# Optimization experiments

Hardware: AMD Instinct MI355X
Metric: run time of the kernel (lower is better)

The kernel has to match this reference:

```python
import jax, jax.numpy as jnp
import numpy as np

B, T, D, H, C = 256, 512, 128, 2048, 128

def setup_inputs() -> dict:
    key = jax.random.key(0)
    ks = jax.random.split(key, 4)
    def xavier(k, shape):
        fan_in, fan_out = shape
        a = jnp.sqrt(6.0 / (fan_in + fan_out))
        return jax.random.uniform(k, shape, jnp.float32, -a, a)
    return {
        "x": jax.random.randint(ks[0], (B, T), 0, D, dtype=jnp.int32),
        "W_hx": xavier(ks[1], (D, H)),
        "W_hh": xavier(ks[2], (H, H)),
        "W_ph": xavier(ks[3], (H, C)),
        "b_h": jnp.zeros((H,), jnp.float32),
        "b_p": jnp.zeros((C,), jnp.float32),
    }

def reference(x, W_hx, W_hh, W_ph, b_h, b_p):
    # one_hot(x) @ W_hx is just a row gather of W_hx (same math, no dense one-hot)
    xw = W_hx[x] + b_h            # [B, T, H]
    xw_t = jnp.swapaxes(xw, 0, 1)  # [T, B, H] for scan over time

    def step(h, xw_step):
        h_new = jnp.tanh(xw_step + h @ W_hh)
        return h_new, None

    h0 = jnp.zeros((B, H), xw.dtype)
    h_final, _ = jax.lax.scan(step, h0, xw_t)
    out = h_final @ W_ph + b_p    # [B, C]
    return out
```

## Files before the change

### kernel.cpp

```cpp
#include <hip/hip_runtime.h>
#include <hip/hip_fp16.h>

#define B_ 256
#define T_ 512
#define H_ 2048
#define C_ 128
#define ASTR 520
#define BSTR2 1030
#define POLLCAP 200000

#define WS_H0 (0u)
#define WS_H1 (1u << 20)
#define WS_BT (2u << 20)

typedef _Float16 half8 __attribute__((ext_vector_type(8)));
typedef float floatx4 __attribute__((ext_vector_type(4)));

__device__ unsigned g_sync[8192];
__device__ _Float16 g_fb[2][8][32][H_];


__device__ __forceinline__ half8 llc_load16(const _Float16* p) {
    union { unsigned long long u[2]; half8 h; } v;
    const unsigned long long* q = (const unsigned long long*)p;
    v.u[0] = __hip_atomic_load(q,     __ATOMIC_RELAXED, __HIP_MEMORY_SCOPE_AGENT);
    v.u[1] = __hip_atomic_load(q + 1, __ATOMIC_RELAXED, __HIP_MEMORY_SCOPE_AGENT);
    return v.h;
}

__device__ __forceinline__ int xcc_id() {
    int x;
    asm volatile("s_getreg_b32 %0, hwreg(HW_REG_XCC_ID)" : "=s"(x));
    return x & 7;
}

__device__ __forceinline__ void flag_inc(unsigned* p) {
    __hip_atomic_fetch_add(p, 1u, __ATOMIC_RELAXED, __HIP_MEMORY_SCOPE_AGENT);
}
__device__ __forceinline__ void flag_poll_ge(const unsigned* p, unsigned tgt) {
    int n = 0;
    while (__hip_atomic_load(p, __ATOMIC_RELAXED, __HIP_MEMORY_SCOPE_AGENT) < tgt
           && n < POLLCAP) { __builtin_amdgcn_s_sleep(2); ++n; }
}

__global__ void convert_whh(const float* __restrict__ W, _Float16* __restrict__ BT) {
    __shared__ float tile[64][65];
    const int kb = blockIdx.x * 64, nb = blockIdx.y * 64;
    const int tid = threadIdx.x;
    const int rc = tid & 63, rr = tid >> 6;
#pragma unroll
    for (int i = 0; i < 16; ++i)
        tile[i * 4 + rr][rc] = W[(size_t)(kb + i * 4 + rr) * H_ + nb + rc];
    __syncthreads();
    const int j = tid & 15, blk = (tid >> 4) & 1, nof = tid >> 5;
#pragma unroll
    for (int i = 0; i < 8; ++i) {
        int n = i * 8 + nof;
        _Float16 v0 = (_Float16)tile[blk * 32 + j][n];
        _Float16 v1 = (_Float16)tile[blk * 32 + 16 + j][n];
        unsigned pk = ((unsigned)__builtin_bit_cast(unsigned short, v1) << 16)
                    |  (unsigned)__builtin_bit_cast(unsigned short, v0);
        *(unsigned*)(BT + (size_t)(nb + n) * H_ + kb + blk * 32 + 2 * j) = pk;
    }
}

__global__ void init_h(const int* __restrict__ x, const float* __restrict__ W_hx,
                       const float* __restrict__ b_h, char* __restrict__ ws) {
    int idx = blockIdx.x * blockDim.x + threadIdx.x;
    if (idx < 8192) g_sync[idx] = 0;
    _Float16* h0 = (_Float16*)(ws + WS_H0);
    int b = idx >> 11, s = idx & (H_ - 1);
    int j = (s & ~31) + ((s & 31) >> 1) + ((s & 1) << 4);
    int xv = x[b * T_];
    h0[idx] = (_Float16)tanhf(W_hx[(size_t)xv * H_ + j] + b_h[j]);
}

#define AL(dst, blk) { const _Float16* _ab = ap + (blk) * 256;              \
    _Pragma("unroll") for (int u = 0; u < 8; ++u)                           \
        asm volatile("global_load_dwordx4 %0, %1, off offset:%2 sc0"        \
                     : "=v"(dst[u]) : "v"(_ab), "i"(u * 64)); }

#define AL2(Aa, Bb0, Bb1, q) {                                              \
    const _Float16* _a2 = ap2 + (q) * 128;                                  \
    const _Float16* _b0 = btp0 + (q) * 128;                                 \
    const _Float16* _b1 = btp1 + (q) * 128;                                 \
    _Pragma("unroll") for (int u = 0; u < 4; ++u)                           \
        asm volatile("global_load_dwordx4 %0, %1, off offset:%2 sc0"        \
                     : "=v"(Aa[u]) : "v"(_a2), "i"(u * 64));                \
    _Pragma("unroll") for (int u = 0; u < 4; ++u)                           \
        asm volatile("global_load_dwordx4 %0, %1, off offset:%2 sc0"        \
                     : "=v"(Bb0[u]) : "v"(_b0), "i"(u * 64));               \
    _Pragma("unroll") for (int u = 0; u < 4; ++u)                           \
        asm volatile("global_load_dwordx4 %0, %1, off offset:%2 sc0"        \
                     : "=v"(Bb1[u]) : "v"(_b1), "i"(u * 64)); }

#define VWAIT(n)                                                            \
    asm volatile("s_waitcnt vmcnt(" #n ")" ::: "memory");                   \
    __builtin_amdgcn_sched_barrier(0);

#define FC_LDS(src, blk)                                                    \
    _Pragma("unroll") for (int u = 0; u < 8; ++u) {                         \
        half8 b0v = *(const half8*)(bsp0 + ((blk) * 8 + u) * 32);           \
        half8 b1v = *(const half8*)(bsp1 + ((blk) * 8 + u) * 32);           \
        acc0 = __builtin_amdgcn_mfma_f32_16x16x32_f16(src[u], b0v, acc0, 0, 0, 0); \
        acc1 = __builtin_amdgcn_mfma_f32_16x16x32_f16(src[u], b1v, acc1, 0, 0, 0); \
    }

#define FC_REG(Aa, Bb0, Bb1)                                                \
    _Pragma("unroll") for (int u = 0; u < 4; ++u) {                         \
        acc0 = __builtin_amdgcn_mfma_f32_16x16x32_f16(Aa[u], Bb0[u], acc0, 0, 0, 0); \
        acc1 = __builtin_amdgcn_mfma_f32_16x16x32_f16(Aa[u], Bb1[u], acc1, 0, 0, 0); \
    }

#define POLLF(qq) {                                                         \
    int guard = 0;                                                          \
    for (;;) {                                                              \
        unsigned fvv = need;                                                \
        if (l < 4) fvv = __hip_atomic_load(&gflags[(rb * 16 + (qq) * 4 + l) * 4], \
                                           __ATOMIC_RELAXED, __HIP_MEMORY_SCOPE_AGENT); \
        if (__ballot(fvv >= need) == ~0ull) break;                          \
        if (++guard > POLLCAP) break;                                       \
        __builtin_amdgcn_s_sleep(2);                                        \
    } }

#define STAGE_LOAD(hb, qq, r) {                                             \
    const _Float16* sp = (hb) + (size_t)(rbr + srow) * H_ + (qq) * 512 + skb; \
    r[0] = llc_load16(sp);      r[1] = llc_load16(sp + 8);                  \
    r[2] = llc_load16(sp + 16); r[3] = llc_load16(sp + 24); }

#define STAGE_WRITE(buf, r) {                                               \
    _Float16* dp = Asl + (buf) * 16 * ASTR + srow * ASTR + skb;             \
    *(half8*)(dp)      = r[0]; *(half8*)(dp + 8)  = r[1];                   \
    *(half8*)(dp + 16) = r[2]; *(half8*)(dp + 24) = r[3]; }

#define COMPUTE(qq) {                                                       \
    const _Float16* ar  = Asl + ((qq) & 1) * 16 * ASTR + l15 * ASTR + kl;   \
    const _Float16* b0p = BT + (size_t)(cw + l15) * H_ + (qq) * 512 + kl;   \
    const _Float16* b1p = BT + (size_t)(cw + 16 + l15) * H_ + (qq) * 512 + kl; \
    _Pragma("unroll")                                                       \
    for (int i = 0; i < 16; ++i) {                                          \
        half8 a  = *(const half8*)(ar  + i * 32);                           \
        half8 b0 = *(const half8*)(b0p + i * 32);                           \
        half8 b1 = *(const half8*)(b1p + i * 32);                           \
        acc0 = __builtin_amdgcn_mfma_f32_16x16x32_f16(a, b0, acc0, 0, 0, 0);\
        acc1 = __builtin_amdgcn_mfma_f32_16x16x32_f16(a, b1, acc1, 0, 0, 0);\
    } }

__global__ __launch_bounds__(256, 1)
void rnn_steps(char* __restrict__ ws, const int* __restrict__ x,
               const float* __restrict__ W_hx, const float* __restrict__ b_h) {
    extern __shared__ _Float16 lds[];
    __shared__ int s_fast, s_wslot;
    _Float16* h0 = (_Float16*)(ws + WS_H0);
    _Float16* h1 = (_Float16*)(ws + WS_H1);
    const _Float16* BT = (const _Float16*)(ws + WS_BT);
    unsigned* census = g_sync;
    unsigned* gflags = g_sync + 4384;

    const int bid = blockIdx.x;
    const int tid = threadIdx.x;
    const int myxcd = xcc_id();

    if (tid == 0) {
        unsigned prev = __hip_atomic_fetch_add(&census[myxcd], 1u, __ATOMIC_RELAXED,
                                               __HIP_MEMORY_SCOPE_AGENT);
        __hip_atomic_fetch_add(&census[8], 1u, __ATOMIC_RELAXED, __HIP_MEMORY_SCOPE_AGENT);
        int p = 0;
        while (__hip_atomic_load(&census[8], __ATOMIC_RELAXED, __HIP_MEMORY_SCOPE_AGENT)
                   < 256u && p < POLLCAP) { __builtin_amdgcn_s_sleep(2); ++p; }
        int ok = (p < POLLCAP);
        if (ok)
            for (int i = 0; i < 8; ++i)
                if (__hip_atomic_load(&census[i], __ATOMIC_RELAXED, __HIP_MEMORY_SCOPE_AGENT)
                        != 32u) { ok = 0; break; }
        s_fast = ok; s_wslot = (int)prev;
    }
    __syncthreads();
    const bool fast = (s_fast != 0);
    const int wslot = s_wslot;

    const int w   = tid >> 6;
    const int l   = tid & 63;
    const int l15 = l & 15;
    const int kl  = (l >> 4) << 3;

    if (fast) {
        const int ns = wslot;
        _Float16* bsf = lds;
        unsigned* scnt = &g_sync[32 + myxcd * 32];

        {
            const int c = tid >> 2, kseg = (tid & 3) * 256;
            const _Float16* src = BT + (size_t)(ns * 64 + c) * H_ + kseg;
            _Float16* dst = bsf + c * BSTR2 + kseg;
#pragma unroll
            for (int i = 0; i < 32; ++i)
                *(half8*)(dst + i * 8) = *(const half8*)(src + i * 8);
        }
        {
            const _Float16* src = h0 + (size_t)(32 * myxcd + ns) * H_ + tid * 8;
            *(half8*)(&g_fb[0][myxcd][ns][tid * 8]) = *(const half8*)(src);
        }
        __syncthreads();
        if (tid == 0) flag_inc(scnt);

        const int mrow = 16 * (w & 1);
        const int cblk = 32 * (w >> 1);
        const int arow = mrow + l15;
        const int r0l  = mrow + ((l >> 4) << 2);
        const int c0   = 64 * ns + cblk + l15;
        const float bh0 = b_h[c0], bh1 = b_h[c0 + 16];
        const _Float16* bsp0 = bsf + (cblk + l15) * BSTR2 + kl;
        const _Float16* bsp1 = bsf + (cblk + 16 + l15) * BSTR2 + kl;
        const _Float16* btp0 = BT + (size_t)c0 * H_ + 1024 + kl;
        const _Float16* btp1 = BT + (size_t)(c0 + 16) * H_ + 1024 + kl;
        const unsigned uofs = (unsigned)(64 * ns + cblk) / 2 + (unsigned)l15;

        for (int t = 1; t < T_; ++t) {
            if (tid == 0) flag_poll_ge(scnt, 32u * (unsigned)t);
            __syncthreads();

            int   xv[4];
            float wx0[4], wx1[4];
#pragma unroll
            for (int jj = 0; jj < 4; ++jj)
                xv[jj] = x[(32 * myxcd + r0l + jj) * T_ + t];
#pragma unroll
            for (int jj = 0; jj < 4; ++jj) {
                wx0[jj] = W_hx[(size_t)xv[jj] * H_ + c0];
                wx1[jj] = W_hx[(size_t)xv[jj] * H_ + c0 + 16];
            }
            asm volatile("" ::: "memory");

            const _Float16* ap  = &g_fb[(t - 1) & 1][myxcd][arow][kl];
            const _Float16* ap2 = ap + 1024;
            floatx4 acc0 = {0.f, 0.f, 0.f, 0.f}, acc1 = {0.f, 0.f, 0.f, 0.f};

            half8 aA[8], aB[8];
            AL(aA, 0); AL(aB, 1);
            VWAIT(8);  FC_LDS(aA, 0);
            AL(aA, 2); VWAIT(8); FC_LDS(aB, 1);
            AL(aB, 3); VWAIT(8); FC_LDS(aA, 2);
            half8 a2A[4], b0A[4], b1A[4], a2B[4], b0B[4], b1B[4];
            AL2(a2A, b0A, b1A, 0);
            VWAIT(12); FC_LDS(aB, 3);
            AL2(a2B, b0B, b1B, 1); VWAIT(12); FC_REG(a2A, b0A, b1A);
            AL2(a2A, b0A, b1A, 2); VWAIT(12); FC_REG(a2B, b0B, b1B);
            AL2(a2B, b0B, b1B, 3); VWAIT(12); FC_REG(a2A, b0A, b1A);
            AL2(a2A, b0A, b1A, 4); VWAIT(12); FC_REG(a2B, b0B, b1B);
            AL2(a2B, b0B, b1B, 5); VWAIT(12); FC_REG(a2A, b0A, b1A);
            AL2(a2A, b0A, b1A, 6); VWAIT(12); FC_REG(a2B, b0B, b1B);
            AL2(a2B, b0B, b1B, 7); VWAIT(12); FC_REG(a2A, b0A, b1A);
            VWAIT(0);  FC_REG(a2B, b0B, b1B);

            _Float16* fbn = &g_fb[t & 1][myxcd][0][0];
#pragma unroll
            for (int jj = 0; jj < 4; ++jj) {
                float z0 = acc0[jj] + wx0[jj] + bh0;
                float z1 = acc1[jj] + wx1[jj] + bh1;
                _Float16 p0 = (_Float16)tanhf(z0), p1 = (_Float16)tanhf(z1);
                unsigned pv = ((unsigned)__builtin_bit_cast(unsigned short, p1) << 16)
                            |  (unsigned)__builtin_bit_cast(unsigned short, p0);
                ((unsigned*)(fbn + (size_t)(r0l + jj) * H_))[uofs] = pv;
                if (t == T_ - 1)
                    ((unsigned*)(h1 + (size_t)(32 * myxcd + r0l + jj) * H_))[uofs] = pv;
            }
            __syncthreads();
            if (tid == 0) flag_inc(scnt);
        }
        return;
    }

    _Float16* Asl = lds;
    const int rb  = bid >> 4;
    const int cb  = bid & 15;
    const int nb  = cb * 128;
    const int cw  = nb + w * 32;
    const int rbr = rb * 16;
    const int srow = tid >> 4;
    const int skb  = (tid & 15) * 32;
    const int r0 = rbr + ((l >> 4) << 2);
    const int c0 = cw + l15;
    const float bh0 = b_h[c0], bh1 = b_h[c0 + 16];
    unsigned* myflag = &gflags[(rb * 16 + cb) * 4];

    for (int t = 1; t < T_; ++t) {
        const _Float16* __restrict__ hc = (t & 1) ? h0 : h1;
        _Float16* __restrict__ hn       = (t & 1) ? h1 : h0;
        const unsigned need = (unsigned)(t - 1);

        int   xv[4];
        float wx0[4], wx1[4];
#pragma unroll
        for (int jj = 0; jj < 4; ++jj) xv[jj] = x[(r0 + jj) * T_ + t];
#pragma unroll
        for (int jj = 0; jj < 4; ++jj) {
            wx0[jj] = W_hx[(size_t)xv[jj] * H_ + c0];
            wx1[jj] = W_hx[(size_t)xv[jj] * H_ + c0 + 16];
        }

        floatx4 acc0 = {0.f, 0.f, 0.f, 0.f}, acc1 = {0.f, 0.f, 0.f, 0.f};
        POLLF(0);
        {
            half8 rA[4];
            STAGE_LOAD(hc, 0, rA);
            STAGE_WRITE(0, rA);
        }
        __syncthreads();
#pragma unroll
        for (int q = 0; q < 4; ++q) {
            half8 rN[4];
            if (q < 3) { POLLF(q + 1); STAGE_LOAD(hc, q + 1, rN); }
            COMPUTE(q);
            if (q < 3) {
                __syncthreads();
                STAGE_WRITE((q + 1) & 1, rN);
                __syncthreads();
            }
        }
        unsigned o[4];
#pragma unroll
        for (int jj = 0; jj < 4; ++jj) {
            float z0 = acc0[jj] + wx0[jj] + bh0;
            float z1 = acc1[jj] + wx1[jj] + bh1;
            _Float16 p0 = (_Float16)tanhf(z0), p1 = (_Float16)tanhf(z1);
            unsigned pv = ((unsigned)__builtin_bit_cast(unsigned short, p1) << 16)
                        |  (unsigned)__builtin_bit_cast(unsigned short, p0);
            unsigned* dstp = (unsigned*)(hn + (size_t)(r0 + jj) * H_ + cw + 2 * l15);
            o[jj] = __hip_atomic_exchange(dstp, pv, __ATOMIC_RELAXED,
                                          __HIP_MEMORY_SCOPE_AGENT);
        }
        asm volatile("" :: "v"(o[0]), "v"(o[1]), "v"(o[2]), "v"(o[3]));
        __syncthreads();
        if (tid == 0) {
            __builtin_amdgcn_fence(__ATOMIC_RELEASE, "workgroup");
            __hip_atomic_fetch_add(myflag, 1u, __ATOMIC_RELAXED, __HIP_MEMORY_SCOPE_AGENT);
        }
    }
}

__global__ void final_proj(const char* __restrict__ ws, const float* __restrict__ W_ph,
                           const float* __restrict__ b_p, float* __restrict__ out) {
    __shared__ float part[C_];
    const _Float16* h = (const _Float16*)(ws + WS_H1);
    const int b  = blockIdx.x;
    const int c  = threadIdx.x & (C_ - 1);
    const int hh = threadIdx.x >> 7;
    const int j0 = hh * (H_ / 2);
    float acc = 0.f;
#pragma unroll 4
    for (int s = j0; s < j0 + H_ / 2; ++s) {
        int k = (s & ~31) + ((s & 31) >> 1) + ((s & 1) << 4);
        acc = fmaf((float)h[(size_t)b * H_ + s], W_ph[k * C_ + c], acc);
    }
    if (hh) part[c] = acc;
    __syncthreads();
    if (!hh) out[b * C_ + c] = acc + part[c] + b_p[c];
}

extern "C" void kernel_launch(void* const* d_in, const int* in_sizes, int n_in,
                              void* d_out, int out_size, void* d_ws, size_t ws_size,
                              hipStream_t stream) {
    const int*   x    = (const int*)d_in[0];
    const float* W_hx = (const float*)d_in[1];
    const float* W_hh = (const float*)d_in[2];
    const float* W_ph = (const float*)d_in[3];
    const float* b_h  = (const float*)d_in[4];
    const float* b_p  = (const float*)d_in[5];
    float* out = (float*)d_out;
    char* ws = (char*)d_ws;

    convert_whh<<<dim3(H_ / 64, H_ / 64), 256, 0, stream>>>(W_hh, (_Float16*)(ws + WS_BT));
    init_h<<<(B_ * H_) / 256, 256, 0, stream>>>(x, W_hx, b_h, ws);

    const int smem = 64 * BSTR2 * 2;
    (void)hipFuncSetAttribute((const void*)rnn_steps,
                              hipFuncAttributeMaxDynamicSharedMemorySize, smem);

    char* pws = ws;
    const int* px = x; const float* pwhx = W_hx; const float* pbh = b_h;
    void* args[] = {(void*)&pws, (void*)&px, (void*)&pwhx, (void*)&pbh};
    hipError_t e = hipLaunchCooperativeKernel((void*)rnn_steps, dim3(256), dim3(256),
                                              args, smem, stream);
    if (e != hipSuccess) {
        rnn_steps<<<dim3(256), dim3(256), smem, stream>>>(pws, px, pwhx, pbh);
    }

    final_proj<<<B_, 256, 0, stream>>>(ws, W_ph, b_p, out);
}
```

Measured before the change: 9.639 ms.

## Remap warp tiling to share B fragments across row halves, prepack W_hh tail

The per-XCD recurrent step changes warp tiling. Each warp now covers a 32-row by 16-column tile instead of 16x32, so one B fragment feeds two MFMAs over the low and high row halves. The upper-K half of W_hh is repacked into a lane-contiguous layout (g_pk) by a new pre-kernel, so B loads become coalesced and no longer need the sc0 bypass. The A loads of the hidden state roughly double per warp, since both row halves are loaded, and the pipeline is rebuilt as three rotating register buffers. Output stores become 16-bit scattered writes instead of packed 32-bit writes.

Measured after the change: 8.792 ms. 1.1x faster.

```diff
diff --git a/kernel.cpp b/kernel.cpp
--- a/kernel.cpp
+++ b/kernel.cpp
@@ -18,6 +18,7 @@
 
 __device__ unsigned g_sync[8192];
 __device__ _Float16 g_fb[2][8][32][H_];
+__device__ _Float16 g_pk[2097152];
 
 
 __device__ __forceinline__ half8 llc_load16(const _Float16* p) {
@@ -62,6 +63,18 @@
                     |  (unsigned)__builtin_bit_cast(unsigned short, v0);
         *(unsigned*)(BT + (size_t)(nb + n) * H_ + kb + blk * 32 + 2 * j) = pk;
     }
+}
+
+__global__ void pack_bt(const _Float16* __restrict__ BT) {
+    int idx = blockIdx.x * blockDim.x + threadIdx.x;
+    const int l  = idx & 63;
+    const int u  = (idx >> 6) & 3;
+    const int q  = (idx >> 8) & 7;
+    const int w  = (idx >> 11) & 3;
+    const int ns = idx >> 13;
+    const int col = 64 * ns + 16 * w + (l & 15);
+    const int kb  = 1024 + q * 128 + u * 32 + 8 * (l >> 4);
+    *(half8*)(g_pk + (size_t)idx * 8) = *(const half8*)(BT + (size_t)col * H_ + kb);
 }
 
 __global__ void init_h(const int* __restrict__ x, const float* __restrict__ W_hx,
@@ -75,41 +88,37 @@
     h0[idx] = (_Float16)tanhf(W_hx[(size_t)xv * H_ + j] + b_h[j]);
 }
 
-#define AL(dst, blk) { const _Float16* _ab = ap + (blk) * 256;              \
-    _Pragma("unroll") for (int u = 0; u < 8; ++u)                           \
-        asm volatile("global_load_dwordx4 %0, %1, off offset:%2 sc0"        \
-                     : "=v"(dst[u]) : "v"(_ab), "i"(u * 64)); }
-
-#define AL2(Aa, Bb0, Bb1, q) {                                              \
-    const _Float16* _a2 = ap2 + (q) * 128;                                  \
-    const _Float16* _b0 = btp0 + (q) * 128;                                 \
-    const _Float16* _b1 = btp1 + (q) * 128;                                 \
-    _Pragma("unroll") for (int u = 0; u < 4; ++u)                           \
-        asm volatile("global_load_dwordx4 %0, %1, off offset:%2 sc0"        \
-                     : "=v"(Aa[u]) : "v"(_a2), "i"(u * 64));                \
-    _Pragma("unroll") for (int u = 0; u < 4; ++u)                           \
-        asm volatile("global_load_dwordx4 %0, %1, off offset:%2 sc0"        \
-                     : "=v"(Bb0[u]) : "v"(_b0), "i"(u * 64));               \
-    _Pragma("unroll") for (int u = 0; u < 4; ++u)                           \
-        asm volatile("global_load_dwordx4 %0, %1, off offset:%2 sc0"        \
-                     : "=v"(Bb1[u]) : "v"(_b1), "i"(u * 64)); }
-
 #define VWAIT(n)                                                            \
     asm volatile("s_waitcnt vmcnt(" #n ")" ::: "memory");                   \
     __builtin_amdgcn_sched_barrier(0);
 
-#define FC_LDS(src, blk)                                                    \
-    _Pragma("unroll") for (int u = 0; u < 8; ++u) {                         \
-        half8 b0v = *(const half8*)(bsp0 + ((blk) * 8 + u) * 32);           \
-        half8 b1v = *(const half8*)(bsp1 + ((blk) * 8 + u) * 32);           \
-        acc0 = __builtin_amdgcn_mfma_f32_16x16x32_f16(src[u], b0v, acc0, 0, 0, 0); \
-        acc1 = __builtin_amdgcn_mfma_f32_16x16x32_f16(src[u], b1v, acc1, 0, 0, 0); \
-    }
-
-#define FC_REG(Aa, Bb0, Bb1)                                                \
+#define ALD(BL, BH, q) {                                                    \
+    const _Float16* _aL = apL + (q) * 128;                                  \
+    const _Float16* _aH = apH + (q) * 128;                                  \
+    _Pragma("unroll") for (int u = 0; u < 4; ++u)                           \
+        asm volatile("global_load_dwordx4 %0, %1, off offset:%2 sc0"        \
+                     : "=v"(BL[u]) : "v"(_aL), "i"(u * 64));                \
+    _Pragma("unroll") for (int u = 0; u < 4; ++u)                           \
+        asm volatile("global_load_dwordx4 %0, %1, off offset:%2 sc0"        \
+                     : "=v"(BH[u]) : "v"(_aH), "i"(u * 64)); }
+
+#define BLD(BB, qp) {                                                       \
+    const _Float16* _bp = pkp + (qp) * 2048;                                \
+    _Pragma("unroll") for (int u = 0; u < 4; ++u)                           \
+        asm volatile("global_load_dwordx4 %0, %1, off offset:%2"            \
+                     : "=v"(BB[u]) : "v"(_bp), "i"(u * 1024)); }
+
+#define CP_LDS(BL, BH, q)                                                   \
     _Pragma("unroll") for (int u = 0; u < 4; ++u) {                         \
-        acc0 = __builtin_amdgcn_mfma_f32_16x16x32_f16(Aa[u], Bb0[u], acc0, 0, 0, 0); \
-        acc1 = __builtin_amdgcn_mfma_f32_16x16x32_f16(Aa[u], Bb1[u], acc1, 0, 0, 0); \
+        half8 bv = *(const half8*)(bsp + (q) * 128 + u * 32);               \
+        acc0 = __builtin_amdgcn_mfma_f32_16x16x32_f16(BL[u], bv, acc0, 0, 0, 0); \
+        acc1 = __builtin_amdgcn_mfma_f32_16x16x32_f16(BH[u], bv, acc1, 0, 0, 0); \
+    }
+
+#define CP_REG(BL, BH, BB)                                                  \
+    _Pragma("unroll") for (int u = 0; u < 4; ++u) {                         \
+        acc0 = __builtin_amdgcn_mfma_f32_16x16x32_f16(BL[u], BB[u], acc0, 0, 0, 0); \
+        acc1 = __builtin_amdgcn_mfma_f32_16x16x32_f16(BH[u], BB[u], acc1, 0, 0, 0); \
     }
 
 #define POLLF(qq) {                                                         \
@@ -204,66 +213,68 @@
         __syncthreads();
         if (tid == 0) flag_inc(scnt);
 
-        const int mrow = 16 * (w & 1);
-        const int cblk = 32 * (w >> 1);
-        const int arow = mrow + l15;
-        const int r0l  = mrow + ((l >> 4) << 2);
-        const int c0   = 64 * ns + cblk + l15;
-        const float bh0 = b_h[c0], bh1 = b_h[c0 + 16];
-        const _Float16* bsp0 = bsf + (cblk + l15) * BSTR2 + kl;
-        const _Float16* bsp1 = bsf + (cblk + 16 + l15) * BSTR2 + kl;
-        const _Float16* btp0 = BT + (size_t)c0 * H_ + 1024 + kl;
-        const _Float16* btp1 = BT + (size_t)(c0 + 16) * H_ + 1024 + kl;
-        const unsigned uofs = (unsigned)(64 * ns + cblk) / 2 + (unsigned)l15;
+        const int r0l = (l >> 4) << 2;
+        const int c0  = 64 * ns + 16 * w + l15;
+        const float bh = b_h[c0];
+        const _Float16* bsp = bsf + (16 * w + l15) * BSTR2 + kl;
+        const _Float16* pkp = g_pk + (size_t)(ns * 4 + w) * 16384 + l * 8;
+        const int blk32 = 2 * ns + (w >> 1);
+        const int selem = blk32 * 32 + ((w & 1) ? (2 * l15 + 1) : (2 * l15));
 
         for (int t = 1; t < T_; ++t) {
             if (tid == 0) flag_poll_ge(scnt, 32u * (unsigned)t);
             __syncthreads();
 
-            int   xv[4];
-            float wx0[4], wx1[4];
-#pragma unroll
-            for (int jj = 0; jj < 4; ++jj)
-                xv[jj] = x[(32 * myxcd + r0l + jj) * T_ + t];
+            int   xv[8];
+            float wx[8];
 #pragma unroll
             for (int jj = 0; jj < 4; ++jj) {
-                wx0[jj] = W_hx[(size_t)xv[jj] * H_ + c0];
-                wx1[jj] = W_hx[(size_t)xv[jj] * H_ + c0 + 16];
+                xv[jj]     = x[(32 * myxcd + r0l + jj) * T_ + t];
+                xv[4 + jj] = x[(32 * myxcd + 16 + r0l + jj) * T_ + t];
             }
+#pragma unroll
+            for (int jj = 0; jj < 8; ++jj)
+                wx[jj] = W_hx[(size_t)xv[jj] * H_ + c0];
             asm volatile("" ::: "memory");
 
-            const _Float16* ap  = &g_fb[(t - 1) & 1][myxcd][arow][kl];
-            const _Float16* ap2 = ap + 1024;
+            const _Float16* fbp = &g_fb[(t - 1) & 1][myxcd][0][0];
+            const _Float16* apL = fbp + (size_t)l15 * H_ + kl;
+            const _Float16* apH = fbp + (size_t)(16 + l15) * H_ + kl;
             floatx4 acc0 = {0.f, 0.f, 0.f, 0.f}, acc1 = {0.f, 0.f, 0.f, 0.f};
-
-            half8 aA[8], aB[8];
-            AL(aA, 0); AL(aB, 1);
-            VWAIT(8);  FC_LDS(aA, 0);
-            AL(aA, 2); VWAIT(8); FC_LDS(aB, 1);
-            AL(aB, 3); VWAIT(8); FC_LDS(aA, 2);
-            half8 a2A[4], b0A[4], b1A[4], a2B[4], b0B[4], b1B[4];
-            AL2(a2A, b0A, b1A, 0);
-            VWAIT(12); FC_LDS(aB, 3);
-            AL2(a2B, b0B, b1B, 1); VWAIT(12); FC_REG(a2A, b0A, b1A);
-            AL2(a2A, b0A, b1A, 2); VWAIT(12); FC_REG(a2B, b0B, b1B);
-            AL2(a2B, b0B, b1B, 3); VWAIT(12); FC_REG(a2A, b0A, b1A);
-            AL2(a2A, b0A, b1A, 4); VWAIT(12); FC_REG(a2B, b0B, b1B);
-            AL2(a2B, b0B, b1B, 5); VWAIT(12); FC_REG(a2A, b0A, b1A);
-            AL2(a2A, b0A, b1A, 6); VWAIT(12); FC_REG(a2B, b0B, b1B);
-            AL2(a2B, b0B, b1B, 7); VWAIT(12); FC_REG(a2A, b0A, b1A);
-            VWAIT(0);  FC_REG(a2B, b0B, b1B);
+            half8 XL[4], XH[4], YL[4], YH[4], ZL[4], ZH[4];
+            half8 BXr[4], BYr[4], BZr[4];
+
+            ALD(XL, XH, 0); ALD(YL, YH, 1);
+            VWAIT(8);  ALD(ZL, ZH, 2);             CP_LDS(XL, XH, 0);
+            VWAIT(8);  ALD(XL, XH, 3);             CP_LDS(YL, YH, 1);
+            VWAIT(8);  ALD(YL, YH, 4);             CP_LDS(ZL, ZH, 2);
+            VWAIT(8);  ALD(ZL, ZH, 5);             CP_LDS(XL, XH, 3);
+            VWAIT(8);  ALD(XL, XH, 6);             CP_LDS(YL, YH, 4);
+            VWAIT(8);  ALD(YL, YH, 7);             CP_LDS(ZL, ZH, 5);
+            VWAIT(8);  ALD(ZL, ZH, 8);  BLD(BZr, 0); CP_LDS(XL, XH, 6);
+            VWAIT(8);  ALD(XL, XH, 9);  BLD(BXr, 1); CP_LDS(YL, YH, 7);
+            VWAIT(12); ALD(YL, YH, 10); BLD(BYr, 2); CP_REG(ZL, ZH, BZr);
+            VWAIT(12); ALD(ZL, ZH, 11); BLD(BZr, 3); CP_REG(XL, XH, BXr);
+            VWAIT(12); ALD(XL, XH, 12); BLD(BXr, 4); CP_REG(YL, YH, BYr);
+            VWAIT(12); ALD(YL, YH, 13); BLD(BYr, 5); CP_REG(ZL, ZH, BZr);
+            VWAIT(12); ALD(ZL, ZH, 14); BLD(BZr, 6); CP_REG(XL, XH, BXr);
+            VWAIT(12); ALD(XL, XH, 15); BLD(BXr, 7); CP_REG(YL, YH, BYr);
+            VWAIT(12);                               CP_REG(ZL, ZH, BZr);
+            VWAIT(0);                                CP_REG(XL, XH, BXr);
 
             _Float16* fbn = &g_fb[t & 1][myxcd][0][0];
 #pragma unroll
             for (int jj = 0; jj < 4; ++jj) {
-                float z0 = acc0[jj] + wx0[jj] + bh0;
-                float z1 = acc1[jj] + wx1[jj] + bh1;
-                _Float16 p0 = (_Float16)tanhf(z0), p1 = (_Float16)tanhf(z1);
-                unsigned pv = ((unsigned)__builtin_bit_cast(unsigned short, p1) << 16)
-                            |  (unsigned)__builtin_bit_cast(unsigned short, p0);
-                ((unsigned*)(fbn + (size_t)(r0l + jj) * H_))[uofs] = pv;
-                if (t == T_ - 1)
-                    ((unsigned*)(h1 + (size_t)(32 * myxcd + r0l + jj) * H_))[uofs] = pv;
+                float zL = acc0[jj] + wx[jj]     + bh;
+                float zH = acc1[jj] + wx[4 + jj] + bh;
+                _Float16 pL = (_Float16)tanhf(zL);
+                _Float16 pH = (_Float16)tanhf(zH);
+                fbn[(size_t)(r0l + jj) * H_ + selem]      = pL;
+                fbn[(size_t)(16 + r0l + jj) * H_ + selem] = pH;
+                if (t == T_ - 1) {
+                    h1[(size_t)(32 * myxcd + r0l + jj) * H_ + selem]      = pL;
+                    h1[(size_t)(32 * myxcd + 16 + r0l + jj) * H_ + selem] = pH;
+                }
             }
             __syncthreads();
             if (tid == 0) flag_inc(scnt);
@@ -371,6 +382,7 @@
     char* ws = (char*)d_ws;
 
     convert_whh<<<dim3(H_ / 64, H_ / 64), 256, 0, stream>>>(W_hh, (_Float16*)(ws + WS_BT));
+    pack_bt<<<1024, 256, 0, stream>>>((const _Float16*)(ws + WS_BT));
     init_h<<<(B_ * H_) / 256, 256, 0, stream>>>(x, W_hx, b_h, ws);
 
     const int smem = 64 * BSTR2 * 2;
```
